# Optimization experiments

Measured on AMD Instinct MI355X. Metric: run time of the kernel, lower is better.

Reference implementation:

```python
import jax, jax.numpy as jnp
import numpy as np

N, K, D = 65536, 1024, 256


def setup_inputs() -> dict:
    key = jax.random.key(0)
    k1, k2 = jax.random.split(key)
    input_data = jax.random.normal(k1, (N, D), dtype=jnp.float32)
    codebooks = jax.random.normal(k2, (K, D), dtype=jnp.float32)
    return {"input_data": input_data, "codebooks": codebooks}


def reference(input_data, codebooks):
    # Squared Euclidean distances [N, K] via the expanded form
    # in the torch source, without the [N, D, K] intermediate).
    x_sq = jnp.sum(input_data * input_data, axis=-1, keepdims=True)      # [N, 1]
    c_sq = jnp.sum(codebooks * codebooks, axis=-1)                       # [K]
    distances = x_sq + c_sq[None, :] - 2.0 * (input_data @ codebooks.T)  # [N, K]

    min_indices = jnp.argmin(distances, axis=1)                          # [N]
    quantized_input = codebooks[min_indices]                             # [N, D]

    loss = jnp.mean(jnp.square(input_data - quantized_input))

    # avg_probs = mean over rows of one_hot(min_indices, K) == counts / N
    counts = jnp.zeros((K,), dtype=jnp.float32).at[min_indices].add(1.0)
    avg_probs = counts / jnp.float32(N)
    perplexity = jnp.exp(-jnp.sum(avg_probs * jnp.log(avg_probs + 1e-10)))

    return quantized_input, loss, perplexity, min_indices
```

## Files before the change

### kernel.cpp

```cpp
#include <hip/hip_runtime.h>
#include <math.h>

#define N_ROWS 65536
#define K_CODES 1024
#define D_DIM 256
#define TAU 0.12f

#define WS_NFLAG   0
#define WS_CSQ     16
#define WS_COUNTS  4112
#define WS_MINIDX  8208
#define WS_LIST    270352
#define WS_PART    532496
#define WS_CSQD    536592
#define WS_CBH     544784

typedef _Float16 f16x8 __attribute__((ext_vector_type(8)));
typedef float    f32x4 __attribute__((ext_vector_type(4)));

__device__ __forceinline__ void gl_lds16(const _Float16* g, _Float16* l) {
    __builtin_amdgcn_global_load_lds(
        (const __attribute__((address_space(1))) unsigned int*)g,
        (__attribute__((address_space(3))) unsigned int*)l, 16, 0, 0);
}

__global__ __launch_bounds__(256) void k_prep(
    const float* __restrict__ cb, _Float16* __restrict__ cbh,
    float* __restrict__ csq, double* __restrict__ csqd,
    float* __restrict__ cbT, unsigned* __restrict__ counts,
    unsigned* __restrict__ nflag)
{
    const int b2 = blockIdx.x;
    const int t = threadIdx.x;
    const long idx8 = (long)b2 * 2048 + t * 8;
    float4 v0 = *(const float4*)(cb + idx8);
    float4 v1 = *(const float4*)(cb + idx8 + 4);
    f16x8 h;
    h[0] = (_Float16)v0.x; h[1] = (_Float16)v0.y; h[2] = (_Float16)v0.z; h[3] = (_Float16)v0.w;
    h[4] = (_Float16)v1.x; h[5] = (_Float16)v1.y; h[6] = (_Float16)v1.z; h[7] = (_Float16)v1.w;
    *(f16x8*)(cbh + idx8) = h;
    {
        const int row = b2 * 8 + (t >> 5);
        const int col = (t & 31) * 8;
        cbT[(col + 0) * 1024 + row] = v0.x;
        cbT[(col + 1) * 1024 + row] = v0.y;
        cbT[(col + 2) * 1024 + row] = v0.z;
        cbT[(col + 3) * 1024 + row] = v0.w;
        cbT[(col + 4) * 1024 + row] = v1.x;
        cbT[(col + 5) * 1024 + row] = v1.y;
        cbT[(col + 6) * 1024 + row] = v1.z;
        cbT[(col + 7) * 1024 + row] = v1.w;
    }
    double sqd = (double)v0.x * v0.x + (double)v0.y * v0.y
               + (double)v0.z * v0.z + (double)v0.w * v0.w
               + (double)v1.x * v1.x + (double)v1.y * v1.y
               + (double)v1.z * v1.z + (double)v1.w * v1.w;
    for (int off = 16; off > 0; off >>= 1) sqd += __shfl_down(sqd, off, 32);
    if ((t & 31) == 0) {
        csqd[b2 * 8 + (t >> 5)] = sqd;
        csq[b2 * 8 + (t >> 5)] = (float)sqd;
    }
    if (b2 < 4) counts[b2 * 256 + t] = 0u;
    if (b2 == 0 && t == 0) *nflag = 0u;
}

__device__ __forceinline__ void merge2(float& m1, int& i1, float& m2,
                                       float om1, int oi1, float om2) {
    float hi  = fmaxf(m1, om1);
    float lo2 = fminf(m2, om2);
    bool take = (om1 < m1) || (om1 == m1 && oi1 < i1);
    if (take) { m1 = om1; i1 = oi1; }
    m2 = fminf(hi, lo2);
}

__global__ __launch_bounds__(256, 2) void k_main(
    const float* __restrict__ x, const _Float16* __restrict__ cbh,
    const float* __restrict__ csq,
    int* __restrict__ min_idx, int* __restrict__ list,
    unsigned* __restrict__ nflag, double* __restrict__ partials)
{
    __shared__ __attribute__((aligned(16))) _Float16 Bs[2][128 * 64];
    __shared__ float  xsq_s[128];
    __shared__ double wred[4];

    const int tid  = threadIdx.x;
    const int w    = tid >> 6;
    const int lane = tid & 63;
    const int rlow = lane & 15;
    const int quad = lane >> 4;
    const long n0  = (long)blockIdx.x * 128;

#pragma unroll
    for (int r = 0; r < 4; ++r) {
        int o = r * 256 + tid;
        int row = o >> 3, s = o & 7, g = s ^ (row & 7);
        gl_lds16(cbh + (long)row * 256 + g * 8, Bs[0] + o * 8);
    }

    f16x8 a_reg[8][2];
#pragma unroll
    for (int i = 0; i < 2; ++i) {
        float cs[8];
        const float* rp = x + (n0 + w * 32 + i * 16 + rlow) * 256;
#pragma unroll
        for (int c = 0; c < 8; ++c) {
            const float* src = rp + c * 32 + quad * 8;
            float4 v0 = *(const float4*)src;
            float4 v1 = *(const float4*)(src + 4);
            f16x8 h;
            h[0] = (_Float16)v0.x; h[1] = (_Float16)v0.y; h[2] = (_Float16)v0.z; h[3] = (_Float16)v0.w;
            h[4] = (_Float16)v1.x; h[5] = (_Float16)v1.y; h[6] = (_Float16)v1.z; h[7] = (_Float16)v1.w;
            a_reg[c][i] = h;
            cs[c] = v0.x * v0.x + v0.y * v0.y + v0.z * v0.z + v0.w * v0.w
                  + v1.x * v1.x + v1.y * v1.y + v1.z * v1.z + v1.w * v1.w;
        }
        float s1_0 = cs[0] + cs[4], s1_1 = cs[1] + cs[5];
        float s1_2 = cs[2] + cs[6], s1_3 = cs[3] + cs[7];
        float s2_0 = s1_0 + s1_2, s2_1 = s1_1 + s1_3;
        float s3 = s2_0 + s2_1;
        float s4 = s3 + __shfl_down(s3, 32, 64);
        float s5 = s4 + __shfl_down(s4, 16, 64);
        if (quad == 0) xsq_s[w * 32 + i * 16 + rlow] = s5;
    }

    float sm1[8], sm2[8];
    int   si1[8];
#pragma unroll
    for (int s = 0; s < 8; s++) { sm1[s] = INFINITY; sm2[s] = INFINITY; si1[s] = 0; }

    f32x4 acc[16];
    const f32x4 z = {0.f, 0.f, 0.f, 0.f};
#pragma unroll
    for (int t2 = 0; t2 < 16; t2++) acc[t2] = z;

    __syncthreads();

    for (int kt = 0; kt < 8; ++kt) {
#pragma unroll
        for (int dblk = 0; dblk < 4; ++dblk) {
            const int cur = dblk & 1;
            if (dblk != 3 || kt != 7) {
                const int  ktn = (dblk == 3) ? kt + 1 : kt;
                const int  d0  = ((dblk + 1) & 3) * 64;
                _Float16* dst = Bs[cur ^ 1];
#pragma unroll
                for (int r = 0; r < 4; ++r) {
                    int o = r * 256 + tid;
                    int row = o >> 3, s = o & 7, g = s ^ (row & 7);
                    gl_lds16(cbh + ((long)ktn * 128 + row) * 256 + d0 + g * 8,
                             dst + o * 8);
                }
            }
            const _Float16* B = Bs[cur];
#pragma unroll
            for (int h = 0; h < 2; ++h) {
                f16x8 b[8];
#pragma unroll
                for (int j = 0; j < 8; ++j) {
                    int row = j * 16 + rlow;
                    int s = (h * 4 + quad) ^ (rlow & 7);
                    b[j] = *(const f16x8*)&B[row * 64 + s * 8];
                }
#pragma unroll
                for (int i = 0; i < 2; ++i)
#pragma unroll
                    for (int j = 0; j < 8; ++j)
                        acc[i * 8 + j] = __builtin_amdgcn_mfma_f32_16x16x32_f16(
                            a_reg[dblk * 2 + h][i], b[j], acc[i * 8 + j], 0, 0, 0);
            }
            if (dblk == 3) {
                const int kbase = kt * 128;
#pragma unroll
                for (int j = 0; j < 8; ++j) {
                    const int code = kbase + j * 16 + rlow;
                    const float csj = csq[code];
#pragma unroll
                    for (int i = 0; i < 2; ++i)
#pragma unroll
                        for (int v = 0; v < 4; ++v) {
                            const int s = i * 4 + v;
                            float val = fmaf(-2.f, acc[i * 8 + j][v], csj);
                            bool lt = val < sm1[s];
                            sm2[s] = fminf(fmaxf(val, sm1[s]), sm2[s]);
                            si1[s] = lt ? code : si1[s];
                            sm1[s] = fminf(val, sm1[s]);
                        }
                }
#pragma unroll
                for (int t2 = 0; t2 < 16; ++t2) acc[t2] = z;
            }
            __syncthreads();
        }
    }

#pragma unroll
    for (int s = 0; s < 8; ++s) {
#pragma unroll
        for (int m = 1; m < 16; m <<= 1) {
            float om1 = __shfl_xor(sm1[s], m, 64);
            float om2 = __shfl_xor(sm2[s], m, 64);
            int   oi1 = __shfl_xor(si1[s], m, 64);
            merge2(sm1[s], si1[s], sm2[s], om1, oi1, om2);
        }
    }

    double lsum = 0.0;
    if (rlow == 0) {
#pragma unroll
        for (int i = 0; i < 2; ++i)
#pragma unroll
            for (int v = 0; v < 4; ++v) {
                const int s = i * 4 + v;
                const int rl = w * 32 + i * 16 + quad * 4 + v;
                const long n = n0 + rl;
                min_idx[n] = si1[s];
                if (sm2[s] - sm1[s] < TAU) {
                    unsigned pp = atomicAdd(nflag, 1u);
                    list[pp] = (int)n;
                }
                lsum += (double)xsq_s[rl] + (double)sm1[s];
            }
    }
    lsum += __shfl_down(lsum, 32, 64);
    lsum += __shfl_down(lsum, 16, 64);
    if (lane == 0) wred[w] = lsum;
    __syncthreads();
    if (tid == 0) partials[blockIdx.x] = ((wred[0] + wred[1]) + wred[2]) + wred[3];
}

#define RPB 2
__global__ __launch_bounds__(256) void k_refine(
    const float* __restrict__ x, const float* __restrict__ cbT,
    const double* __restrict__ csqd, const unsigned* __restrict__ nflag,
    const int* __restrict__ list, int* __restrict__ min_idx)
{
    __shared__ double xsd[RPB][256];
    __shared__ double rbv[RPB][4];
    __shared__ int    rbi[RPB][4];
    const int tid = threadIdx.x;
    const int w = tid >> 6, lane = tid & 63;
    const unsigned nf = *nflag;
    const int k0 = tid * 4;

    for (unsigned base = blockIdx.x * RPB; base < nf; base += gridDim.x * RPB) {
        __syncthreads();
#pragma unroll
        for (int r = 0; r < RPB; ++r) {
            unsigned it = base + r; if (it > nf - 1) it = nf - 1;
            int ridx = list[it];
            xsd[r][tid] = (double)x[(long)ridx * D_DIM + tid];
        }
        __syncthreads();

        double s0[RPB], s1[RPB], s2[RPB], s3[RPB];
#pragma unroll
        for (int r = 0; r < RPB; ++r) { s0[r] = 0.0; s1[r] = 0.0; s2[r] = 0.0; s3[r] = 0.0; }

#pragma unroll 4
        for (int d = 0; d < D_DIM; ++d) {
            float4 c = *(const float4*)(cbT + d * 1024 + k0);
            double c0 = (double)c.x, c1 = (double)c.y;
            double c2 = (double)c.z, c3 = (double)c.w;
#pragma unroll
            for (int r = 0; r < RPB; ++r) {
                double xv = xsd[r][d];
                s0[r] = fma(xv, c0, s0[r]);
                s1[r] = fma(xv, c1, s1[r]);
                s2[r] = fma(xv, c2, s2[r]);
                s3[r] = fma(xv, c3, s3[r]);
            }
        }

        double best[RPB]; int bidx[RPB];
#pragma unroll
        for (int r = 0; r < RPB; ++r) { best[r] = 1e300; bidx[r] = 0; }
        {
            const double ck0 = csqd[k0];
            const double ck1 = csqd[k0 + 1];
            const double ck2 = csqd[k0 + 2];
            const double ck3 = csqd[k0 + 3];
#pragma unroll
            for (int r = 0; r < RPB; ++r) {
                double dd;
                dd = fma(-2.0, s0[r], ck0);
                if (dd < best[r] || (dd == best[r] && k0 < bidx[r])) { best[r] = dd; bidx[r] = k0; }
                dd = fma(-2.0, s1[r], ck1);
                if (dd < best[r] || (dd == best[r] && k0 + 1 < bidx[r])) { best[r] = dd; bidx[r] = k0 + 1; }
                dd = fma(-2.0, s2[r], ck2);
                if (dd < best[r] || (dd == best[r] && k0 + 2 < bidx[r])) { best[r] = dd; bidx[r] = k0 + 2; }
                dd = fma(-2.0, s3[r], ck3);
                if (dd < best[r] || (dd == best[r] && k0 + 3 < bidx[r])) { best[r] = dd; bidx[r] = k0 + 3; }
            }
        }

#pragma unroll
        for (int r = 0; r < RPB; ++r) {
            double bv = best[r]; int bi = bidx[r];
            for (int off = 32; off > 0; off >>= 1) {
                double od = __shfl_down(bv, off, 64);
                int    oi = __shfl_down(bi, off, 64);
                if (od < bv || (od == bv && oi < bi)) { bv = od; bi = oi; }
            }
            if (lane == 0) { rbv[r][w] = bv; rbi[r][w] = bi; }
        }
        __syncthreads();
        if (tid < RPB && base + tid < nf) {
            double bb = rbv[tid][0]; int bi_ = rbi[tid][0];
#pragma unroll
            for (int wv = 1; wv < 4; ++wv) {
                if (rbv[tid][wv] < bb || (rbv[tid][wv] == bb && rbi[tid][wv] < bi_)) {
                    bb = rbv[tid][wv]; bi_ = rbi[tid][wv];
                }
            }
            min_idx[list[base + tid]] = bi_;
        }
    }
}

__global__ __launch_bounds__(256) void k_out(
    const float* __restrict__ cb, const int* __restrict__ min_idx,
    float* __restrict__ out, unsigned* __restrict__ counts)
{
    const int tid  = threadIdx.x;
    const int wave = tid >> 6;
    const int lane = tid & 63;
    const long n = (long)blockIdx.x * 4 + wave;
    const int idx = min_idx[n];

    float4 q = *(const float4*)(cb + (long)idx * D_DIM + lane * 4);
    *(float4*)(out + n * D_DIM + lane * 4) = q;

    if (lane == 0) {
        atomicAdd(&counts[idx], 1u);
        out[16777218L + n] = (float)idx;
    }
}

__global__ void k_final(const double* __restrict__ partials,
                        const unsigned* __restrict__ counts, float* __restrict__ out)
{
    __shared__ double red[256];
    const int tid = threadIdx.x;

    red[tid] = partials[tid] + partials[tid + 256];
    __syncthreads();
    for (int off = 128; off > 0; off >>= 1) { if (tid < off) red[tid] += red[tid + off]; __syncthreads(); }
    double loss = red[0] / (double)((long)N_ROWS * D_DIM);
    __syncthreads();

    double h = 0.0;
    for (int k = tid; k < K_CODES; k += 256) {
        double p = (double)counts[k] / (double)N_ROWS;
        h += p * log(p + 1e-10);
    }
    red[tid] = h;
    __syncthreads();
    for (int off = 128; off > 0; off >>= 1) { if (tid < off) red[tid] += red[tid + off]; __syncthreads(); }

    if (tid == 0) {
        out[16777216] = (float)loss;
        out[16777217] = (float)exp(-red[0]);
    }
}

extern "C" void kernel_launch(void* const* d_in, const int* in_sizes, int n_in,
                              void* d_out, int out_size, void* d_ws, size_t ws_size,
                              hipStream_t stream)
{
    const float* x  = (const float*)d_in[0];
    const float* cb = (const float*)d_in[1];
    float* out = (float*)d_out;
    char*  ws  = (char*)d_ws;

    unsigned*  nflag    = (unsigned*)(ws + WS_NFLAG);
    float*     csq      = (float*)(ws + WS_CSQ);
    unsigned*  counts   = (unsigned*)(ws + WS_COUNTS);
    int*       min_idx  = (int*)(ws + WS_MINIDX);
    int*       list     = (int*)(ws + WS_LIST);
    double*    partials = (double*)(ws + WS_PART);
    double*    csqd     = (double*)(ws + WS_CSQD);
    _Float16*  cbh      = (_Float16*)(ws + WS_CBH);
    float*     cbT      = out + 8781824L;

    hipLaunchKernelGGL(k_prep,   dim3(128),  dim3(256), 0, stream,
                       cb, cbh, csq, csqd, cbT, counts, nflag);
    hipLaunchKernelGGL(k_main,   dim3(512),  dim3(256), 0, stream,
                       x, cbh, csq, min_idx, list, nflag, partials);
    hipLaunchKernelGGL(k_refine, dim3(1024), dim3(256), 0, stream,
                       x, cbT, csqd, nflag, list, min_idx);
    hipLaunchKernelGGL(k_out,    dim3(N_ROWS / 4), dim3(256), 0, stream,
                       cb, min_idx, out, counts);
    hipLaunchKernelGGL(k_final,  dim3(1), dim3(256), 0, stream, partials, counts, out);
}
```

Before: 224.5 us.

## Deepen codebook LDS pipeline to four stages with explicit vmcnt waits

Expands the shared-memory codebook buffer from two to four stages and prefetches two d-blocks ahead instead of one. The full __syncthreads is replaced by counted s_waitcnt vmcnt plus a bare s_barrier, so only the tile about to be consumed must have landed. The per-tile accumulator zeroing is folded into the first MFMA, which now takes a zero accumulator. This aims to hide global-load latency and cut barrier stalls, at the cost of doubling LDS use, which may reduce occupancy, and of relying on hand-tuned wait counts that must match the number of outstanding loads.

```diff
diff --git a/kernel.cpp b/kernel.cpp
--- a/kernel.cpp
+++ b/kernel.cpp
@@ -79,7 +79,7 @@
     int* __restrict__ min_idx, int* __restrict__ list,
     unsigned* __restrict__ nflag, double* __restrict__ partials)
 {
-    __shared__ __attribute__((aligned(16))) _Float16 Bs[2][128 * 64];
+    __shared__ __attribute__((aligned(16))) _Float16 Bs[4][128 * 64];
     __shared__ float  xsq_s[128];
     __shared__ double wred[4];
 
@@ -95,6 +95,12 @@
         int o = r * 256 + tid;
         int row = o >> 3, s = o & 7, g = s ^ (row & 7);
         gl_lds16(cbh + (long)row * 256 + g * 8, Bs[0] + o * 8);
+    }
+#pragma unroll
+    for (int r = 0; r < 4; ++r) {
+        int o = r * 256 + tid;
+        int row = o >> 3, s = o & 7, g = s ^ (row & 7);
+        gl_lds16(cbh + (long)row * 256 + 64 + g * 8, Bs[1] + o * 8);
     }
 
     f16x8 a_reg[8][2];
@@ -138,20 +144,31 @@
     for (int kt = 0; kt < 8; ++kt) {
 #pragma unroll
         for (int dblk = 0; dblk < 4; ++dblk) {
-            const int cur = dblk & 1;
-            if (dblk != 3 || kt != 7) {
-                const int  ktn = (dblk == 3) ? kt + 1 : kt;
-                const int  d0  = ((dblk + 1) & 3) * 64;
-                _Float16* dst = Bs[cur ^ 1];
+            if (kt < 7 || dblk < 2) {
+                const int ktn = (dblk >= 2) ? kt + 1 : kt;
+                const int d0n = ((dblk + 2) & 3) * 64;
+                _Float16* dst = Bs[(dblk + 2) & 3];
 #pragma unroll
                 for (int r = 0; r < 4; ++r) {
                     int o = r * 256 + tid;
                     int row = o >> 3, s = o & 7, g = s ^ (row & 7);
-                    gl_lds16(cbh + ((long)ktn * 128 + row) * 256 + d0 + g * 8,
+                    gl_lds16(cbh + ((long)ktn * 128 + row) * 256 + d0n + g * 8,
                              dst + o * 8);
                 }
             }
-            const _Float16* B = Bs[cur];
+            if (dblk == 2) {
+                if (kt == 7) asm volatile("s_waitcnt vmcnt(4)" ::: "memory");
+                else         asm volatile("s_waitcnt vmcnt(8)" ::: "memory");
+            } else if (dblk == 3) {
+                if (kt == 7) asm volatile("s_waitcnt vmcnt(0)" ::: "memory");
+                else         asm volatile("s_waitcnt vmcnt(8)" ::: "memory");
+            } else {
+                asm volatile("s_waitcnt vmcnt(8)" ::: "memory");
+            }
+            __builtin_amdgcn_s_barrier();
+            __builtin_amdgcn_sched_barrier(0);
+
+            const _Float16* B = Bs[dblk];
 #pragma unroll
             for (int h = 0; h < 2; ++h) {
                 f16x8 b[8];
@@ -164,9 +181,14 @@
 #pragma unroll
                 for (int i = 0; i < 2; ++i)
 #pragma unroll
-                    for (int j = 0; j < 8; ++j)
-                        acc[i * 8 + j] = __builtin_amdgcn_mfma_f32_16x16x32_f16(
-                            a_reg[dblk * 2 + h][i], b[j], acc[i * 8 + j], 0, 0, 0);
+                    for (int j = 0; j < 8; ++j) {
+                        if (dblk == 0 && h == 0)
+                            acc[i * 8 + j] = __builtin_amdgcn_mfma_f32_16x16x32_f16(
+                                a_reg[0][i], b[j], z, 0, 0, 0);
+                        else
+                            acc[i * 8 + j] = __builtin_amdgcn_mfma_f32_16x16x32_f16(
+                                a_reg[dblk * 2 + h][i], b[j], acc[i * 8 + j], 0, 0, 0);
+                    }
             }
             if (dblk == 3) {
                 const int kbase = kt * 128;
@@ -186,10 +208,7 @@
                             sm1[s] = fminf(val, sm1[s]);
                         }
                 }
-#pragma unroll
-                for (int t2 = 0; t2 < 16; ++t2) acc[t2] = z;
-            }
-            __syncthreads();
+            }
         }
     }
 
```

New measurement: 224.9 us. About the same (+0.2%).

## Split codebook search across two blocks per row tile and merge partial minima

Applied to the files above, without the earlier changes.

Each 128-row tile is now handled by two blocks, each scanning half of the 1024 codes, which doubles the grid to 1024 blocks. The per-half top-2 minima and indices are written to scratch space inside the output buffer, and a new merge kernel combines them, flags near-tie rows for refinement and reduces the loss partials. It also caches code norms in LDS, folds the accumulator zeroing into the first MFMA, and raises launch bounds to 4 waves per SIMD. The aim is more parallelism and occupancy on the main GEMM-argmin, at the cost of recomputing the x fp16 conversion twice, an extra kernel launch and extra global traffic.

```diff
diff --git a/kernel.cpp b/kernel.cpp
--- a/kernel.cpp
+++ b/kernel.cpp
@@ -73,29 +73,33 @@
     m2 = fminf(hi, lo2);
 }
 
-__global__ __launch_bounds__(256, 2) void k_main(
+__global__ __launch_bounds__(256, 4) void k_main(
     const float* __restrict__ x, const _Float16* __restrict__ cbh,
     const float* __restrict__ csq,
-    int* __restrict__ min_idx, int* __restrict__ list,
-    unsigned* __restrict__ nflag, double* __restrict__ partials)
+    float* __restrict__ m1h, float* __restrict__ m2h, float* __restrict__ i1f,
+    float* __restrict__ xsqg)
 {
     __shared__ __attribute__((aligned(16))) _Float16 Bs[2][128 * 64];
-    __shared__ float  xsq_s[128];
-    __shared__ double wred[4];
+    __shared__ __attribute__((aligned(16))) float csq_s[512];
+    __shared__ float xsq_s[128];
 
     const int tid  = threadIdx.x;
     const int w    = tid >> 6;
     const int lane = tid & 63;
     const int rlow = lane & 15;
     const int quad = lane >> 4;
-    const long n0  = (long)blockIdx.x * 128;
+    const int rowTile = blockIdx.x >> 1;
+    const int half    = blockIdx.x & 1;
+    const long n0  = (long)rowTile * 128;
+    const int khalf = half * 512;
 
 #pragma unroll
     for (int r = 0; r < 4; ++r) {
         int o = r * 256 + tid;
         int row = o >> 3, s = o & 7, g = s ^ (row & 7);
-        gl_lds16(cbh + (long)row * 256 + g * 8, Bs[0] + o * 8);
-    }
+        gl_lds16(cbh + (long)(khalf + row) * 256 + g * 8, Bs[0] + o * 8);
+    }
+    if (tid < 128) *(float4*)&csq_s[tid * 4] = *(const float4*)&csq[khalf + tid * 4];
 
     f16x8 a_reg[8][2];
 #pragma unroll
@@ -135,19 +139,19 @@
 
     __syncthreads();
 
-    for (int kt = 0; kt < 8; ++kt) {
+    for (int kt = 0; kt < 4; ++kt) {
 #pragma unroll
         for (int dblk = 0; dblk < 4; ++dblk) {
             const int cur = dblk & 1;
-            if (dblk != 3 || kt != 7) {
-                const int  ktn = (dblk == 3) ? kt + 1 : kt;
-                const int  d0  = ((dblk + 1) & 3) * 64;
+            if (dblk != 3 || kt != 3) {
+                const int ktn = (dblk == 3) ? kt + 1 : kt;
+                const int d0  = ((dblk + 1) & 3) * 64;
                 _Float16* dst = Bs[cur ^ 1];
 #pragma unroll
                 for (int r = 0; r < 4; ++r) {
                     int o = r * 256 + tid;
                     int row = o >> 3, s = o & 7, g = s ^ (row & 7);
-                    gl_lds16(cbh + ((long)ktn * 128 + row) * 256 + d0 + g * 8,
+                    gl_lds16(cbh + ((long)(khalf + ktn * 128) + row) * 256 + d0 + g * 8,
                              dst + o * 8);
                 }
             }
@@ -164,16 +168,22 @@
 #pragma unroll
                 for (int i = 0; i < 2; ++i)
 #pragma unroll
-                    for (int j = 0; j < 8; ++j)
-                        acc[i * 8 + j] = __builtin_amdgcn_mfma_f32_16x16x32_f16(
-                            a_reg[dblk * 2 + h][i], b[j], acc[i * 8 + j], 0, 0, 0);
+                    for (int j = 0; j < 8; ++j) {
+                        if (dblk == 0 && h == 0)
+                            acc[i * 8 + j] = __builtin_amdgcn_mfma_f32_16x16x32_f16(
+                                a_reg[0][i], b[j], z, 0, 0, 0);
+                        else
+                            acc[i * 8 + j] = __builtin_amdgcn_mfma_f32_16x16x32_f16(
+                                a_reg[dblk * 2 + h][i], b[j], acc[i * 8 + j], 0, 0, 0);
+                    }
             }
             if (dblk == 3) {
                 const int kbase = kt * 128;
 #pragma unroll
                 for (int j = 0; j < 8; ++j) {
-                    const int code = kbase + j * 16 + rlow;
-                    const float csj = csq[code];
+                    const int cloc = kbase + j * 16 + rlow;
+                    const int code = khalf + cloc;
+                    const float csj = csq_s[cloc];
 #pragma unroll
                     for (int i = 0; i < 2; ++i)
 #pragma unroll
@@ -186,8 +196,6 @@
                             sm1[s] = fminf(val, sm1[s]);
                         }
                 }
-#pragma unroll
-                for (int t2 = 0; t2 < 16; ++t2) acc[t2] = z;
             }
             __syncthreads();
         }
@@ -204,28 +212,51 @@
         }
     }
 
-    double lsum = 0.0;
     if (rlow == 0) {
+        const long hb = (long)half * 65536;
 #pragma unroll
         for (int i = 0; i < 2; ++i)
 #pragma unroll
             for (int v = 0; v < 4; ++v) {
                 const int s = i * 4 + v;
-                const int rl = w * 32 + i * 16 + quad * 4 + v;
-                const long n = n0 + rl;
-                min_idx[n] = si1[s];
-                if (sm2[s] - sm1[s] < TAU) {
-                    unsigned pp = atomicAdd(nflag, 1u);
-                    list[pp] = (int)n;
-                }
-                lsum += (double)xsq_s[rl] + (double)sm1[s];
-            }
-    }
-    lsum += __shfl_down(lsum, 32, 64);
-    lsum += __shfl_down(lsum, 16, 64);
-    if (lane == 0) wred[w] = lsum;
+                const long n = n0 + w * 32 + i * 16 + quad * 4 + v;
+                m1h[hb + n] = sm1[s];
+                m2h[hb + n] = sm2[s];
+                i1f[hb + n] = (float)si1[s];
+            }
+    }
+    if (half == 0 && tid < 128) xsqg[n0 + tid] = xsq_s[tid];
+}
+
+__global__ __launch_bounds__(256) void k_merge(
+    const float* __restrict__ m1h, const float* __restrict__ m2h,
+    const float* __restrict__ i1f, const float* __restrict__ xsq,
+    int* __restrict__ min_idx, int* __restrict__ list,
+    unsigned* __restrict__ nflag, double* __restrict__ partials)
+{
+    __shared__ double red[256];
+    const int tid = threadIdx.x;
+    const int n = blockIdx.x * 256 + tid;
+
+    float m1a = m1h[n], m1b = m1h[65536 + n];
+    float m2a = m2h[n], m2b = m2h[65536 + n];
+    int   ia  = (int)i1f[n], ib = (int)i1f[65536 + n];
+
+    bool bw = (m1b < m1a) || (m1b == m1a && ib < ia);
+    float m1 = bw ? m1b : m1a;
+    int   i1 = bw ? ib : ia;
+    float m2 = fminf(bw ? m1a : m1b, bw ? m2b : m2a);
+
+    min_idx[n] = i1;
+    if (m2 - m1 < TAU) { unsigned p = atomicAdd(nflag, 1u); list[p] = n; }
+
+    red[tid] = (double)xsq[n] + (double)m1;
     __syncthreads();
-    if (tid == 0) partials[blockIdx.x] = ((wred[0] + wred[1]) + wred[2]) + wred[3];
+    for (int off = 128; off > 0; off >>= 1) {
+        if (tid < off) red[tid] += red[tid + off];
+        __syncthreads();
+    }
+    if (tid == 0) partials[blockIdx.x] = red[0];
 }
 
 #define RPB 2
@@ -342,7 +373,7 @@
     __shared__ double red[256];
     const int tid = threadIdx.x;
 
-    red[tid] = partials[tid] + partials[tid + 256];
+    red[tid] = partials[tid];
     __syncthreads();
     for (int off = 128; off > 0; off >>= 1) { if (tid < off) red[tid] += red[tid + off]; __syncthreads(); }
     double loss = red[0] / (double)((long)N_ROWS * D_DIM);
@@ -381,11 +412,17 @@
     double*    csqd     = (double*)(ws + WS_CSQD);
     _Float16*  cbh      = (_Float16*)(ws + WS_CBH);
     float*     cbT      = out + 8781824L;
+    float*     m1h      = out + 9043968L;
+    float*     m2h      = out + 9175040L;
+    float*     i1f      = out + 9306112L;
+    float*     xsqg     = out + 9437184L;
 
     hipLaunchKernelGGL(k_prep,   dim3(128),  dim3(256), 0, stream,
                        cb, cbh, csq, csqd, cbT, counts, nflag);
-    hipLaunchKernelGGL(k_main,   dim3(512),  dim3(256), 0, stream,
-                       x, cbh, csq, min_idx, list, nflag, partials);
+    hipLaunchKernelGGL(k_main,   dim3(1024), dim3(256), 0, stream,
+                       x, cbh, csq, m1h, m2h, i1f, xsqg);
+    hipLaunchKernelGGL(k_merge,  dim3(256),  dim3(256), 0, stream,
+                       m1h, m2h, i1f, xsqg, min_idx, list, nflag, partials);
     hipLaunchKernelGGL(k_refine, dim3(1024), dim3(256), 0, stream,
                        x, cbT, csqd, nflag, list, min_idx);
     hipLaunchKernelGGL(k_out,    dim3(N_ROWS / 4), dim3(256), 0, stream,
```

New measurement: 315.0 us. 1.4x slower.
